# Performance work log

Hardware: AMD Instinct MI355X
Metric: run time of the kernel (lower is better)

## Reference

```python
import jax, jax.numpy as jnp
import numpy as np

D = 1024      # d_model
H = 16        # n_heads
HD = D // H   # head_dim = 64
SQ = 1024     # seq_len_q
SKV = 1024    # seq_len_kv
B = 4
MAXL = max(SQ, SKV)  # max_len of relative positional encoding
SCALE = 1.0 / np.sqrt(HD).astype(np.float32)


def setup_inputs() -> dict:
    key = jax.random.key(0)
    ks = jax.random.split(key, 8)
    s = 0.02
    return {
        "query": jax.random.normal(ks[0], (B, SQ, D), dtype=jnp.float32),
        "key_value": jax.random.normal(ks[1], (B, SKV, D), dtype=jnp.float32),
        "Wq": jax.random.normal(ks[2], (D, D), dtype=jnp.float32) * s,
        "bq": jnp.zeros((D,), dtype=jnp.float32),
        "Wk": jax.random.normal(ks[3], (D, D), dtype=jnp.float32) * s,
        "bk": jnp.zeros((D,), dtype=jnp.float32),
        "Wv": jax.random.normal(ks[4], (D, D), dtype=jnp.float32) * s,
        "bv": jnp.zeros((D,), dtype=jnp.float32),
        "Wo": jax.random.normal(ks[5], (D, D), dtype=jnp.float32) * s,
        "bo": jnp.zeros((D,), dtype=jnp.float32),
        # nn.Parameter(torch.randn(2*max_len-1, head_dim))
        "rel_table": jax.random.normal(ks[6], (2 * MAXL - 1, HD), dtype=jnp.float32),
    }


def reference(query, key_value, Wq, bq, Wk, bk, Wv, bv, Wo, bo, rel_table):
    b = query.shape[0]
    q = query.reshape(b, SQ, D)
    kv = key_value.reshape(b, SKV, D)
    # projections, then split heads -> [b, H, S, HD]
    Q = (q @ Wq + bq).reshape(b, SQ, H, HD).transpose(0, 2, 1, 3)
    K = (kv @ Wk + bk).reshape(b, SKV, H, HD).transpose(0, 2, 1, 3)
    V = (kv @ Wv + bv).reshape(b, SKV, H, HD).transpose(0, 2, 1, 3)
    # content scores
    scores = jnp.einsum('bhid,bhjd->bhij', Q, K) * SCALE
    # relative position bias: rel_pos[i,j] = clip(i-j+MAXL-1, 0, 2*MAXL-2)
    i = jnp.arange(SQ)[:, None]
    j = jnp.arange(SKV)[None, :]
    idx = jnp.clip(i - j + MAXL - 1, 0, 2 * MAXL - 2)
    rel = rel_table[idx]  # [SQ, SKV, HD]
    scores = scores + jnp.einsum('bhid,ijd->bhij', Q, rel)
    attn = jax.nn.softmax(scores, axis=-1)  # dropout is identity in eval
    out = jnp.einsum('bhij,bhjd->bhid', attn, V)
    out = out.transpose(0, 2, 1, 3).reshape(b, SQ, D)
    out = out @ Wo + bo
    return out.reshape(b, -1)
```

## Files before the change

### kernel.cpp

```cpp
#include <hip/hip_runtime.h>
#include <hip/hip_bf16.h>
#include <stdint.h>


typedef __attribute__((ext_vector_type(8))) short short8;
typedef __attribute__((ext_vector_type(4))) float f32x4;

constexpr int Bz = 4, SQv = 1024, SKVv = 1024, Dv = 1024, Hv = 16, HDv = 64;
constexpr float LOG2E = 1.4426950408889634f;
constexpr float C1 = 0.125f * LOG2E;
constexpr float THR2 = 11.5f;

constexpr size_t OFF_QB  = 0;
constexpr size_t OFF_KVB = 8388608;
constexpr size_t OFF_WQT = 16777216;
constexpr size_t OFF_WKT = 18874368;
constexpr size_t OFF_WVT = 20971520;
constexpr size_t OFF_WOT = 23068672;
constexpr size_t OFF_REL = 25165824;
constexpr size_t OFF_Q   = 25427968;
constexpr size_t OFF_K   = 33816576;
constexpr size_t OFF_V   = 42205184;
constexpr size_t OFF_AO  = 50593792;

__device__ __forceinline__ unsigned short f2bf(float f) {
  union { float f; unsigned int u; } v; v.f = f;
  unsigned int r = (v.u + 0x7fffu + ((v.u >> 16) & 1u)) >> 16;
  return (unsigned short)r;
}

__device__ __forceinline__ unsigned short cvtpk1(float x) {
  unsigned int r;
  asm("v_cvt_pk_bf16_f32 %0, %1, %1" : "=v"(r) : "v"(x));
  return (unsigned short)r;
}

__device__ __forceinline__ void gload_lds16(const unsigned short* g, unsigned short* l) {
  __builtin_amdgcn_global_load_lds(
      (const __attribute__((address_space(1))) unsigned int*)g,
      (__attribute__((address_space(3))) unsigned int*)l, 16, 0, 0);
}

template <int CTRL>
__device__ __forceinline__ float dpp_ror(float v) {
  int x = __builtin_amdgcn_update_dpp(__builtin_bit_cast(int, v),
                                      __builtin_bit_cast(int, v),
                                      CTRL, 0xf, 0xf, false);
  return __builtin_bit_cast(float, x);
}
__device__ __forceinline__ float red16_max(float v) {
  v = fmaxf(v, dpp_ror<0x121>(v));
  v = fmaxf(v, dpp_ror<0x122>(v));
  v = fmaxf(v, dpp_ror<0x124>(v));
  v = fmaxf(v, dpp_ror<0x128>(v));
  return v;
}
__device__ __forceinline__ float red16_sum(float v) {
  v += dpp_ror<0x121>(v);
  v += dpp_ror<0x122>(v);
  v += dpp_ror<0x124>(v);
  v += dpp_ror<0x128>(v);
  return v;
}

__global__ __launch_bounds__(256) void k_prep(const float* __restrict__ q,
                                              const float* __restrict__ kv,
                                              const float* __restrict__ rel,
                                              const float* __restrict__ Wq,
                                              const float* __restrict__ Wk,
                                              const float* __restrict__ Wv,
                                              const float* __restrict__ Wo,
                                              unsigned short* __restrict__ qb,
                                              unsigned short* __restrict__ kvb,
                                              unsigned short* __restrict__ relb,
                                              unsigned short* __restrict__ Wqt,
                                              unsigned short* __restrict__ Wkt,
                                              unsigned short* __restrict__ Wvt,
                                              unsigned short* __restrict__ Wot) {
  __shared__ unsigned short t[64][72];
  const int bx = blockIdx.x;
  if (bx < 4096) {
    const float* s = bx < 2048 ? q : kv;
    unsigned short* d = bx < 2048 ? qb : kvb;
    const int base = (bx & 2047) * 2048 + threadIdx.x * 8;
    float4 f0 = *(const float4*)(s + base);
    float4 f1 = *(const float4*)(s + base + 4);
    unsigned short o[8] = {f2bf(f0.x), f2bf(f0.y), f2bf(f0.z), f2bf(f0.w),
                           f2bf(f1.x), f2bf(f1.y), f2bf(f1.z), f2bf(f1.w)};
    *(uint4*)(d + base) = *(const uint4*)o;
    return;
  }
  if (bx < 4160) {
    const int i = (bx - 4096) * 2048 + threadIdx.x * 8;
    const int nsrc = 2047 * 64;
    unsigned short o[8];
    if (i + 8 <= nsrc) {
      float4 f0 = *(const float4*)(rel + i);
      float4 f1 = *(const float4*)(rel + i + 4);
      o[0]=f2bf(f0.x*LOG2E); o[1]=f2bf(f0.y*LOG2E); o[2]=f2bf(f0.z*LOG2E); o[3]=f2bf(f0.w*LOG2E);
      o[4]=f2bf(f1.x*LOG2E); o[5]=f2bf(f1.y*LOG2E); o[6]=f2bf(f1.z*LOG2E); o[7]=f2bf(f1.w*LOG2E);
    } else {
#pragma unroll
      for (int k = 0; k < 8; k++) o[k] = (i + k < nsrc) ? f2bf(rel[i + k]*LOG2E) : (unsigned short)0;
    }
    *(uint4*)(relb + i) = *(const uint4*)o;
    return;
  }
  const int tt = bx - 4160;
  const int z = tt >> 8, tile = tt & 255;
  const float* W = z == 0 ? Wq : z == 1 ? Wk : z == 2 ? Wv : Wo;
  unsigned short* Wt = z == 0 ? Wqt : z == 1 ? Wkt : z == 2 ? Wvt : Wot;
  const int r0 = (tile >> 4) * 64, c0 = (tile & 15) * 64;
  const int tid = threadIdx.x;
  const int r = tid >> 2, cc = (tid & 3) * 16;
  const float* src = W + (size_t)(r0 + r) * Dv + c0 + cc;
#pragma unroll
  for (int i = 0; i < 16; i += 4) {
    float4 f = *(const float4*)(src + i);
    t[r][cc + i + 0] = f2bf(f.x);
    t[r][cc + i + 1] = f2bf(f.y);
    t[r][cc + i + 2] = f2bf(f.z);
    t[r][cc + i + 3] = f2bf(f.w);
  }
  __syncthreads();
  unsigned short tmp[16];
#pragma unroll
  for (int i = 0; i < 16; i++) tmp[i] = t[cc + i][r];
  unsigned short* dstp = Wt + (size_t)(c0 + r) * Dv + r0 + cc;
  *(uint4*)(dstp)     = *(const uint4*)&tmp[0];
  *((uint4*)dstp + 1) = *(const uint4*)&tmp[8];
}

__global__ __launch_bounds__(256) void k_gemm3(const unsigned short* __restrict__ qb,
                                               const unsigned short* __restrict__ kvb,
                                               const unsigned short* __restrict__ Wqt,
                                               const unsigned short* __restrict__ Wkt,
                                               const unsigned short* __restrict__ Wvt,
                                               const float* __restrict__ bq,
                                               const float* __restrict__ bk,
                                               const float* __restrict__ bv,
                                               unsigned short* __restrict__ Qb,
                                               unsigned short* __restrict__ Kb,
                                               unsigned short* __restrict__ Vtb) {
  __shared__ unsigned short As[128 * 32];
  __shared__ unsigned short Bs[128 * 32];
  const int z = blockIdx.z;
  const unsigned short* A  = z == 0 ? qb : kvb;
  const unsigned short* Bt = z == 0 ? Wqt : z == 1 ? Wkt : Wvt;
  const float* bias        = z == 0 ? bq : z == 1 ? bk : bv;
  unsigned short* Cout     = z == 0 ? Qb : z == 1 ? Kb : Vtb;
  const int K = Dv, N = Dv;

  const int tid = threadIdx.x;
  const int l = tid & 63, w = tid >> 6;
  const int wr = w >> 1, wc = w & 1;
  const int m0 = blockIdx.y * 128, n0 = blockIdx.x * 128;
  const int lr = l & 15, kk = (l >> 4) * 8;
  const int srow = tid >> 2, soff = (tid & 3) * 8;

  const unsigned short* Ag = A + (size_t)(m0 + srow) * K + soff;
  const unsigned short* Bg = Bt + (size_t)(n0 + srow) * K + soff;
  unsigned short* AsD = &As[tid * 8];
  unsigned short* BsD = &Bs[tid * 8];

  f32x4 acc[4][4] = {};

  for (int k0 = 0; k0 < K; k0 += 32) {
    __syncthreads();
    gload_lds16(Ag + k0, AsD);
    gload_lds16(Ag + (size_t)64 * K + k0, AsD + 2048);
    gload_lds16(Bg + k0, BsD);
    gload_lds16(Bg + (size_t)64 * K + k0, BsD + 2048);
    __syncthreads();
    short8 af[4], bf[4];
#pragma unroll
    for (int m = 0; m < 4; m++) af[m] = *(const short8*)&As[(wr * 64 + m * 16 + lr) * 32 + kk];
#pragma unroll
    for (int n = 0; n < 4; n++) bf[n] = *(const short8*)&Bs[(wc * 64 + n * 16 + lr) * 32 + kk];
    __builtin_amdgcn_s_setprio(1);
#pragma unroll
    for (int m = 0; m < 4; m++)
#pragma unroll
      for (int n = 0; n < 4; n++)
        acc[m][n] = __builtin_amdgcn_mfma_f32_16x16x32_bf16(af[m], bf[n], acc[m][n], 0, 0, 0);
    __builtin_amdgcn_s_setprio(0);
  }

#pragma unroll
  for (int m = 0; m < 4; m++) {
    const int row_base = m0 + wr * 64 + m * 16 + (l >> 4) * 4;
#pragma unroll
    for (int n = 0; n < 4; n++) {
      const int col = n0 + wc * 64 + n * 16 + lr;
      const float bv4 = bias[col];
      if (z == 2) {
        const int h = col >> 6, hd = col & 63;
        const int bb = row_base >> 10, j = row_base & 1023;
        unsigned short t4[4];
#pragma unroll
        for (int r = 0; r < 4; r++) t4[r] = f2bf(acc[m][n][r] + bv4);
        *(uint2*)&Cout[((size_t)((bb * 16 + h) * 64 + hd)) * 1024 + j] = *(const uint2*)t4;
      } else {
#pragma unroll
        for (int r = 0; r < 4; r++)
          Cout[(size_t)(row_base + r) * N + col] = f2bf(acc[m][n][r] + bv4);
      }
    }
  }
}

__global__ __launch_bounds__(256) void k_gemmO(const unsigned short* __restrict__ A,
                                               const unsigned short* __restrict__ Bt,
                                               const float* __restrict__ bias,
                                               float* __restrict__ Cout) {
  __shared__ unsigned short As[64 * 32];
  __shared__ unsigned short Bs[128 * 32];
  const int K = Dv, N = Dv;
  const int tid = threadIdx.x;
  const int l = tid & 63, w = tid >> 6;
  const int wr = w >> 1, wc = w & 1;
  const int m0 = blockIdx.y * 64, n0 = blockIdx.x * 128;
  const int lr = l & 15, kk = (l >> 4) * 8;
  const int srow = tid >> 2, soff = (tid & 3) * 8;

  const unsigned short* Ag = A + (size_t)(m0 + srow) * K + soff;
  const unsigned short* Bg = Bt + (size_t)(n0 + srow) * K + soff;
  unsigned short* AsD = &As[tid * 8];
  unsigned short* BsD = &Bs[tid * 8];

  f32x4 acc[2][4] = {};

  for (int k0 = 0; k0 < K; k0 += 32) {
    __syncthreads();
    gload_lds16(Ag + k0, AsD);
    gload_lds16(Bg + k0, BsD);
    gload_lds16(Bg + (size_t)64 * K + k0, BsD + 2048);
    __syncthreads();
    short8 af[2], bf[4];
#pragma unroll
    for (int m = 0; m < 2; m++) af[m] = *(const short8*)&As[(wr * 32 + m * 16 + lr) * 32 + kk];
#pragma unroll
    for (int n = 0; n < 4; n++) bf[n] = *(const short8*)&Bs[(wc * 64 + n * 16 + lr) * 32 + kk];
    __builtin_amdgcn_s_setprio(1);
#pragma unroll
    for (int m = 0; m < 2; m++)
#pragma unroll
      for (int n = 0; n < 4; n++)
        acc[m][n] = __builtin_amdgcn_mfma_f32_16x16x32_bf16(af[m], bf[n], acc[m][n], 0, 0, 0);
    __builtin_amdgcn_s_setprio(0);
  }

#pragma unroll
  for (int m = 0; m < 2; m++) {
    const int row_base = m0 + wr * 32 + m * 16 + (l >> 4) * 4;
#pragma unroll
    for (int n = 0; n < 4; n++) {
      const int col = n0 + wc * 64 + n * 16 + lr;
      const float bv4 = bias[col];
#pragma unroll
      for (int r = 0; r < 4; r++)
        Cout[(size_t)(row_base + r) * N + col] = acc[m][n][r] + bv4;
    }
  }
}

__global__ __launch_bounds__(256) void k_attn(const unsigned short* __restrict__ Qb,
                                              const unsigned short* __restrict__ Kb,
                                              const unsigned short* __restrict__ Vt,
                                              const unsigned short* __restrict__ relb,
                                              unsigned short* __restrict__ AO) {
  __shared__ unsigned short Ks[2][64][68];
  __shared__ unsigned short Vs[2][64][68];
  __shared__ float Ts[4][16][66];
  __shared__ unsigned short Ps[4][16][68];

  const int tid = threadIdx.x, l = tid & 63, w = tid >> 6;
  const int lr = l & 15, lg = l >> 4, kk = lg * 8;

  const int raw = blockIdx.x;
  const int work = (raw & 7) * 128 + (raw >> 3);
  const int i0 = (work & 15) * 64;
  const int h = (work >> 4) & 15;
  const int b = work >> 8;

  const unsigned short* Kg  = Kb + (size_t)b * SKVv * Dv + h * HDv;
  const unsigned short* Vtg = Vt + ((size_t)(b * Hv + h) * HDv) * (size_t)SKVv;

  const unsigned short* Qg = Qb + ((size_t)(b * SQv + i0 + w * 16 + lr)) * Dv + h * HDv;
  short8 aq0 = *(const short8*)&Qg[kk];
  short8 aq1 = *(const short8*)&Qg[32 + kk];

  const int sr = tid >> 2, sc = (tid & 3) * 16;

  uint4 pk0, pk1, pv0, pv1;
  auto ldnext = [&](int j0) {
    pk0 = *(const uint4*)&Kg[(size_t)(j0 + sr) * Dv + sc];
    pk1 = *(const uint4*)&Kg[(size_t)(j0 + sr) * Dv + sc + 8];
    pv0 = *(const uint4*)&Vtg[(size_t)sr * SKVv + j0 + sc];
    pv1 = *(const uint4*)&Vtg[(size_t)sr * SKVv + j0 + sc + 8];
  };
  auto wrbuf = [&](int buf) {
    *(uint4*)&Ks[buf][sr][sc]     = pk0;
    *(uint4*)&Ks[buf][sr][sc + 8] = pk1;
    *(uint4*)&Vs[buf][sr][sc]     = pv0;
    *(uint4*)&Vs[buf][sr][sc + 8] = pv1;
  };

  ldnext(0);
  wrbuf(0);
  __syncthreads();

  f32x4 Oacc[4] = {};
  f32x4 vsum[4] = {};
  float mrow[4];
#pragma unroll
  for (int r = 0; r < 4; r++) mrow[r] = -3e38f;

  for (int it = 0; it < 16; ++it) {
    const int cur = it & 1;
    const int j0 = it * 64;
    if (it < 15) ldnext(j0 + 64);

    const int base = i0 - j0 + 960 + w * 16;
    short8 br0[5], br1[5];
#pragma unroll
    for (int tf = 0; tf < 5; tf++) {
      const unsigned short* rp = &relb[(size_t)(base + tf * 16 + lr) * HDv];
      br0[tf] = *(const short8*)&rp[kk];
      br1[tf] = *(const short8*)&rp[32 + kk];
    }

    __builtin_amdgcn_s_setprio(1);
    f32x4 sacc[4] = {};
#pragma unroll
    for (int jf = 0; jf < 4; jf++) {
      short8 bk0 = *(const short8*)&Ks[cur][jf * 16 + lr][kk];
      short8 bk1 = *(const short8*)&Ks[cur][jf * 16 + lr][32 + kk];
      sacc[jf] = __builtin_amdgcn_mfma_f32_16x16x32_bf16(aq0, bk0, sacc[jf], 0, 0, 0);
      sacc[jf] = __builtin_amdgcn_mfma_f32_16x16x32_bf16(aq1, bk1, sacc[jf], 0, 0, 0);
    }

#pragma unroll
    for (int tf = 0; tf < 5; tf++) {
      f32x4 tacc = {};
      tacc = __builtin_amdgcn_mfma_f32_16x16x32_bf16(aq0, br0[tf], tacc, 0, 0, 0);
      tacc = __builtin_amdgcn_mfma_f32_16x16x32_bf16(aq1, br1[tf], tacc, 0, 0, 0);
#pragma unroll
      for (int r = 0; r < 4; r++) {
        const int col = (lg * 4 + r) - (tf * 16 + lr) + 63;
        if ((unsigned)col < 64u) Ts[w][lg * 4 + r][col] = tacc[r];
      }
    }
    __builtin_amdgcn_s_setprio(0);

    float p[4][4], mx4[4];
#pragma unroll
    for (int r = 0; r < 4; r++) {
      const int rr = lg * 4 + r;
#pragma unroll
      for (int jf = 0; jf < 4; jf++)
        p[jf][r] = sacc[jf][r] * C1 + Ts[w][rr][jf * 16 + lr];
      float mx = fmaxf(fmaxf(p[0][r], p[1][r]), fmaxf(p[2][r], p[3][r]));
      mx4[r] = red16_max(mx);
    }
    bool grow = false;
#pragma unroll
    for (int r = 0; r < 4; r++) grow = grow || (mx4[r] > mrow[r] + THR2);
    if (__any(grow ? 1 : 0)) {
#pragma unroll
      for (int r = 0; r < 4; r++) {
        const float mnew = fmaxf(mrow[r], mx4[r]);
        const float rs = __builtin_amdgcn_exp2f(mrow[r] - mnew);
        mrow[r] = mnew;
#pragma unroll
        for (int jf = 0; jf < 4; jf++) vsum[jf][r] *= rs;
#pragma unroll
        for (int df = 0; df < 4; df++) Oacc[df][r] *= rs;
      }
    }
#pragma unroll
    for (int r = 0; r < 4; r++) {
      const int rr = lg * 4 + r;
#pragma unroll
      for (int jf = 0; jf < 4; jf++) {
        const float e = __builtin_amdgcn_exp2f(p[jf][r] - mrow[r]);
        vsum[jf][r] += e;
        Ps[w][rr][jf * 16 + lr] = cvtpk1(e);
      }
    }

    short8 ap0 = *(const short8*)&Ps[w][lr][kk];
    short8 ap1 = *(const short8*)&Ps[w][lr][32 + kk];
    __builtin_amdgcn_s_setprio(1);
#pragma unroll
    for (int df = 0; df < 4; df++) {
      short8 bv0 = *(const short8*)&Vs[cur][df * 16 + lr][kk];
      short8 bv1 = *(const short8*)&Vs[cur][df * 16 + lr][32 + kk];
      Oacc[df] = __builtin_amdgcn_mfma_f32_16x16x32_bf16(ap0, bv0, Oacc[df], 0, 0, 0);
      Oacc[df] = __builtin_amdgcn_mfma_f32_16x16x32_bf16(ap1, bv1, Oacc[df], 0, 0, 0);
    }
    __builtin_amdgcn_s_setprio(0);

    if (it < 15) wrbuf(cur ^ 1);
    __syncthreads();
  }

#pragma unroll
  for (int r = 0; r < 4; r++) {
    float s = vsum[0][r] + vsum[1][r] + vsum[2][r] + vsum[3][r];
    s = red16_sum(s);
    const float inv = 1.f / s;
    const size_t row = (size_t)(b * SQv + i0 + w * 16 + lg * 4 + r) * Dv + h * HDv;
#pragma unroll
    for (int df = 0; df < 4; df++)
      AO[row + df * 16 + lr] = cvtpk1(Oacc[df][r] * inv);
  }
}

extern "C" void kernel_launch(void* const* d_in, const int* in_sizes, int n_in,
                              void* d_out, int out_size, void* d_ws, size_t ws_size,
                              hipStream_t stream) {
  const float* query = (const float*)d_in[0];
  const float* keyv  = (const float*)d_in[1];
  const float* Wq    = (const float*)d_in[2];
  const float* bq    = (const float*)d_in[3];
  const float* Wk    = (const float*)d_in[4];
  const float* bk    = (const float*)d_in[5];
  const float* Wv    = (const float*)d_in[6];
  const float* bv    = (const float*)d_in[7];
  const float* Wo    = (const float*)d_in[8];
  const float* bo    = (const float*)d_in[9];
  const float* rel   = (const float*)d_in[10];

  char* ws = (char*)d_ws;
  unsigned short* qb   = (unsigned short*)(ws + OFF_QB);
  unsigned short* kvb  = (unsigned short*)(ws + OFF_KVB);
  unsigned short* Wqt  = (unsigned short*)(ws + OFF_WQT);
  unsigned short* Wkt  = (unsigned short*)(ws + OFF_WKT);
  unsigned short* Wvt  = (unsigned short*)(ws + OFF_WVT);
  unsigned short* Wot  = (unsigned short*)(ws + OFF_WOT);
  unsigned short* relb = (unsigned short*)(ws + OFF_REL);
  unsigned short* Qb   = (unsigned short*)(ws + OFF_Q);
  unsigned short* Kb   = (unsigned short*)(ws + OFF_K);
  unsigned short* Vtb  = (unsigned short*)(ws + OFF_V);
  unsigned short* AOb  = (unsigned short*)(ws + OFF_AO);

  k_prep<<<5184, 256, 0, stream>>>(query, keyv, rel, Wq, Wk, Wv, Wo,
                                   qb, kvb, relb, Wqt, Wkt, Wvt, Wot);

  dim3 g3(Dv / 128, (Bz * SQv) / 128, 3);
  k_gemm3<<<g3, 256, 0, stream>>>(qb, kvb, Wqt, Wkt, Wvt, bq, bk, bv, Qb, Kb, Vtb);

  k_attn<<<1024, 256, 0, stream>>>(Qb, Kb, Vtb, relb, AOb);

  dim3 go(Dv / 128, (Bz * SQv) / 64);
  k_gemmO<<<go, 256, 0, stream>>>(AOb, Wot, bo, (float*)d_out);
}
```

Measured before the change: 180.7 us.

## Store relative-bias tiles unmasked and gather diagonally, share row max per lane

The relative-position MFMA results are now written to a transposed 80x16 shared buffer with vectorized float2 stores and no per-element bounds checks. The diagonal shift is applied on the read side with an index gather. The running softmax max is collapsed from four per-row values into one per-lane scalar, which drops several reductions and exp2 calls. Global K/V/rel loads now use incrementing pointers instead of recomputed addresses. The shared max across rows is still mathematically valid, but it raises underflow risk when rows in the same group differ widely.

```diff
diff --git a/kernel.cpp b/kernel.cpp
--- a/kernel.cpp
+++ b/kernel.cpp
@@ -271,7 +271,7 @@
                                               unsigned short* __restrict__ AO) {
   __shared__ unsigned short Ks[2][64][68];
   __shared__ unsigned short Vs[2][64][68];
-  __shared__ float Ts[4][16][66];
+  __shared__ float Ts[4][80][18];
   __shared__ unsigned short Ps[4][16][68];
 
   const int tid = threadIdx.x, l = tid & 63, w = tid >> 6;
@@ -292,13 +292,11 @@
 
   const int sr = tid >> 2, sc = (tid & 3) * 16;
 
+  const unsigned short* kld = Kg + (size_t)(64 + sr) * Dv + sc;
+  const unsigned short* vld = Vtg + (size_t)sr * SKVv + 64 + sc;
+  const unsigned short* relit = relb + (size_t)(i0 + 960 + w * 16 + lr) * HDv + kk;
+
   uint4 pk0, pk1, pv0, pv1;
-  auto ldnext = [&](int j0) {
-    pk0 = *(const uint4*)&Kg[(size_t)(j0 + sr) * Dv + sc];
-    pk1 = *(const uint4*)&Kg[(size_t)(j0 + sr) * Dv + sc + 8];
-    pv0 = *(const uint4*)&Vtg[(size_t)sr * SKVv + j0 + sc];
-    pv1 = *(const uint4*)&Vtg[(size_t)sr * SKVv + j0 + sc + 8];
-  };
   auto wrbuf = [&](int buf) {
     *(uint4*)&Ks[buf][sr][sc]     = pk0;
     *(uint4*)&Ks[buf][sr][sc + 8] = pk1;
@@ -306,29 +304,35 @@
     *(uint4*)&Vs[buf][sr][sc + 8] = pv1;
   };
 
-  ldnext(0);
+  pk0 = *(const uint4*)&Kg[(size_t)sr * Dv + sc];
+  pk1 = *(const uint4*)&Kg[(size_t)sr * Dv + sc + 8];
+  pv0 = *(const uint4*)&Vtg[(size_t)sr * SKVv + sc];
+  pv1 = *(const uint4*)&Vtg[(size_t)sr * SKVv + sc + 8];
   wrbuf(0);
   __syncthreads();
 
   f32x4 Oacc[4] = {};
   f32x4 vsum[4] = {};
-  float mrow[4];
-#pragma unroll
-  for (int r = 0; r < 4; r++) mrow[r] = -3e38f;
+  float mrow = -3e38f;
 
   for (int it = 0; it < 16; ++it) {
     const int cur = it & 1;
-    const int j0 = it * 64;
-    if (it < 15) ldnext(j0 + 64);
-
-    const int base = i0 - j0 + 960 + w * 16;
+    if (it < 15) {
+      pk0 = *(const uint4*)&kld[0];
+      pk1 = *(const uint4*)&kld[8];
+      pv0 = *(const uint4*)&vld[0];
+      pv1 = *(const uint4*)&vld[8];
+      kld += (size_t)64 * Dv;
+      vld += 64;
+    }
+
     short8 br0[5], br1[5];
 #pragma unroll
     for (int tf = 0; tf < 5; tf++) {
-      const unsigned short* rp = &relb[(size_t)(base + tf * 16 + lr) * HDv];
-      br0[tf] = *(const short8*)&rp[kk];
-      br1[tf] = *(const short8*)&rp[32 + kk];
-    }
+      br0[tf] = *(const short8*)&relit[(size_t)tf * 16 * HDv];
+      br1[tf] = *(const short8*)&relit[(size_t)tf * 16 * HDv + 32];
+    }
+    relit -= (size_t)64 * HDv;
 
     __builtin_amdgcn_s_setprio(1);
     f32x4 sacc[4] = {};
@@ -345,49 +349,44 @@
       f32x4 tacc = {};
       tacc = __builtin_amdgcn_mfma_f32_16x16x32_bf16(aq0, br0[tf], tacc, 0, 0, 0);
       tacc = __builtin_amdgcn_mfma_f32_16x16x32_bf16(aq1, br1[tf], tacc, 0, 0, 0);
+      float2 t01; t01.x = tacc[0]; t01.y = tacc[1];
+      float2 t23; t23.x = tacc[2]; t23.y = tacc[3];
+      *(float2*)&Ts[w][tf * 16 + lr][4 * lg]     = t01;
+      *(float2*)&Ts[w][tf * 16 + lr][4 * lg + 2] = t23;
+    }
+    __builtin_amdgcn_s_setprio(0);
+
+    float p[4][4];
+#pragma unroll
+    for (int jf = 0; jf < 4; jf++) {
+      const int jj = jf * 16 + lr;
 #pragma unroll
       for (int r = 0; r < 4; r++) {
-        const int col = (lg * 4 + r) - (tf * 16 + lr) + 63;
-        if ((unsigned)col < 64u) Ts[w][lg * 4 + r][col] = tacc[r];
+        const int rr = lg * 4 + r;
+        p[jf][r] = sacc[jf][r] * C1 + Ts[w][rr - jj + 63][rr];
       }
     }
-    __builtin_amdgcn_s_setprio(0);
-
-    float p[4][4], mx4[4];
-#pragma unroll
-    for (int r = 0; r < 4; r++) {
-      const int rr = lg * 4 + r;
-#pragma unroll
-      for (int jf = 0; jf < 4; jf++)
-        p[jf][r] = sacc[jf][r] * C1 + Ts[w][rr][jf * 16 + lr];
-      float mx = fmaxf(fmaxf(p[0][r], p[1][r]), fmaxf(p[2][r], p[3][r]));
-      mx4[r] = red16_max(mx);
-    }
-    bool grow = false;
-#pragma unroll
-    for (int r = 0; r < 4; r++) grow = grow || (mx4[r] > mrow[r] + THR2);
-    if (__any(grow ? 1 : 0)) {
+    float mx = p[0][0];
+#pragma unroll
+    for (int jf = 0; jf < 4; jf++)
+#pragma unroll
+      for (int r = 0; r < 4; r++) mx = fmaxf(mx, p[jf][r]);
+    mx = red16_max(mx);
+    if (__any(mx > mrow + THR2)) {
+      const float mnew = fmaxf(mrow, mx);
+      const float rs = __builtin_amdgcn_exp2f(mrow - mnew);
+      mrow = mnew;
+#pragma unroll
+      for (int q4 = 0; q4 < 4; q4++) { vsum[q4] *= rs; Oacc[q4] *= rs; }
+    }
+#pragma unroll
+    for (int jf = 0; jf < 4; jf++)
 #pragma unroll
       for (int r = 0; r < 4; r++) {
-        const float mnew = fmaxf(mrow[r], mx4[r]);
-        const float rs = __builtin_amdgcn_exp2f(mrow[r] - mnew);
-        mrow[r] = mnew;
-#pragma unroll
-        for (int jf = 0; jf < 4; jf++) vsum[jf][r] *= rs;
-#pragma unroll
-        for (int df = 0; df < 4; df++) Oacc[df][r] *= rs;
+        const float e = __builtin_amdgcn_exp2f(p[jf][r] - mrow);
+        vsum[jf][r] += e;
+        Ps[w][lg * 4 + r][jf * 16 + lr] = cvtpk1(e);
       }
-    }
-#pragma unroll
-    for (int r = 0; r < 4; r++) {
-      const int rr = lg * 4 + r;
-#pragma unroll
-      for (int jf = 0; jf < 4; jf++) {
-        const float e = __builtin_amdgcn_exp2f(p[jf][r] - mrow[r]);
-        vsum[jf][r] += e;
-        Ps[w][rr][jf * 16 + lr] = cvtpk1(e);
-      }
-    }
 
     short8 ap0 = *(const short8*)&Ps[w][lr][kk];
     short8 ap1 = *(const short8*)&Ps[w][lr][32 + kk];
```

After: 174.4 us. 1.04x faster.
